# Kernel tuning notes

Measured on AMD Instinct MI355X. Metric: run time of the kernel, lower is better.

The kernel has to match this reference:

```python
import jax, jax.numpy as jnp
import numpy as np

HIDDEN = 1024
HEADS = 16
HEAD_DIM = HIDDEN // HEADS
EPS = 1e-6


def _layernorm(x, gamma, beta):
    mu = jnp.mean(x, axis=-1, keepdims=True)
    var = jnp.mean(jnp.square(x - mu), axis=-1, keepdims=True)
    return (x - mu) * jax.lax.rsqrt(var + EPS) * gamma + beta


def setup_inputs() -> dict:
    key = jax.random.key(0)
    ks = jax.random.split(key, 16)
    B, S, D = 2, 2048, HIDDEN
    s = 1.0 / np.sqrt(D)
    inp = {
        "x": jax.random.normal(ks[0], (B, S, D), dtype=jnp.float32),
        "Wq": jax.random.uniform(ks[1], (D, D), jnp.float32, -s, s),
        "bq": jnp.zeros((D,), jnp.float32),
        "Wk": jax.random.uniform(ks[2], (D, D), jnp.float32, -s, s),
        "bk": jnp.zeros((D,), jnp.float32),
        "Wv": jax.random.uniform(ks[3], (D, D), jnp.float32, -s, s),
        "bv": jnp.zeros((D,), jnp.float32),
        "Wo": jax.random.uniform(ks[4], (D, D), jnp.float32, -s, s),
        "bo": jnp.zeros((D,), jnp.float32),
        "g1": jnp.ones((D,), jnp.float32),
        "b1": jnp.zeros((D,), jnp.float32),
        "Wup": jax.random.uniform(ks[5], (D, 4 * D), jnp.float32, -s, s),
        "bup": jnp.zeros((4 * D,), jnp.float32),
        "Wdn": jax.random.uniform(ks[6], (4 * D, D), jnp.float32, -0.5 * s, 0.5 * s),
        "bdn": jnp.zeros((D,), jnp.float32),
        "g2": jnp.ones((D,), jnp.float32),
        "b2": jnp.zeros((D,), jnp.float32),
    }
    return inp


def _forward(x, Wq, bq, Wk, bk, Wv, bv, Wo, bo, g1, b1, Wup, bup, Wdn, bdn, g2, b2):
    B, S, D = x.shape
    H, Hd = HEADS, HEAD_DIM
    # projections -> (B, H, S, Hd)
    q = (x @ Wq + bq).reshape(B, S, H, Hd).transpose(0, 2, 1, 3)
    k = (x @ Wk + bk).reshape(B, S, H, Hd).transpose(0, 2, 1, 3)
    v = (x @ Wv + bv).reshape(B, S, H, Hd).transpose(0, 2, 1, 3)
    # full NxN scores (faithful to the source: explicit QK^T, mask, softmax, AV)
    scores = jnp.einsum("bhqd,bhkd->bhqk", q, k) / np.sqrt(Hd)
    causal = jnp.tril(jnp.ones((S, S), dtype=bool))  # (S, S)
    scores = jnp.where(causal, scores, jnp.float32(-1e20))
    attn = jax.nn.softmax(scores, axis=-1)
    # dropout is identity in eval mode
    mid = jnp.einsum("bhqk,bhkd->bqhd", attn, v).reshape(B, S, D)
    attn_out = mid @ Wo + bo
    x = _layernorm(x + attn_out, g1, b1)
    # FFN
    up = jax.nn.relu(x @ Wup + bup)
    down = up @ Wdn + bdn
    return _layernorm(x + down, g2, b2)


def reference(x, Wq, bq, Wk, bk, Wv, bv, Wo, bo, g1, b1, Wup, bup, Wdn, bdn, g2, b2):
    return _forward(x, Wq, bq, Wk, bk, Wv, bv, Wo, bo, g1, b1, Wup, bup, Wdn, bdn, g2, b2)
```

## Files before the change

### kernel.cpp

```cpp
#include <hip/hip_runtime.h>

#define D_MODEL 1024
#define D_FFN   4096
#define SEQ     2048
#define NROWS   4096
#define QKV_LD  3072

typedef __bf16 bf16x8 __attribute__((ext_vector_type(8)));
typedef float  floatx4 __attribute__((ext_vector_type(4)));

#define MFMA_BF16 __builtin_amdgcn_mfma_f32_16x16x32_bf16

__device__ __forceinline__ unsigned short f2bf(float f) {
  unsigned int u = __float_as_uint(f);
  u += 0x7FFFu + ((u >> 16) & 1u);
  return (unsigned short)(u >> 16);
}

template <int C>
__device__ __forceinline__ float ror16(float x) {
  return __int_as_float(
      __builtin_amdgcn_mov_dpp(__float_as_int(x), 0x120 | C, 0xf, 0xf, true));
}

__device__ __forceinline__ void async16(const unsigned short* g, unsigned short* l) {
  __builtin_amdgcn_global_load_lds(
      (const __attribute__((address_space(1))) unsigned int*)g,
      (__attribute__((address_space(3))) unsigned int*)l, 16, 0, 0);
}

__global__ __launch_bounds__(256) void k_prep(
    const float* __restrict__ x,
    const float* __restrict__ Wq, const float* __restrict__ Wk,
    const float* __restrict__ Wv, const float* __restrict__ Wo,
    const float* __restrict__ Wup, const float* __restrict__ Wdn,
    const float* __restrict__ bq, const float* __restrict__ bk,
    const float* __restrict__ bv,
    unsigned short* __restrict__ x_bf, unsigned short* __restrict__ WqkvT,
    unsigned short* __restrict__ WoT, unsigned short* __restrict__ WupT,
    unsigned short* __restrict__ WdnT, float* __restrict__ bqkv) {
  __shared__ float tile[32][33];
  int b = blockIdx.x;
  if (b < 4096) {
    long i = ((long)b * 256 + threadIdx.x) * 4;
    float4 v = *(const float4*)(x + i);
    ushort4 o;
    o.x = f2bf(v.x); o.y = f2bf(v.y); o.z = f2bf(v.z); o.w = f2bf(v.w);
    *(ushort4*)(x_bf + i) = o;
    return;
  }
  if (b >= 16384) {
    int i = (b - 16384) * 256 + threadIdx.x;
    if (i < 3072) {
      float v = (i < 1024) ? bq[i] : (i < 2048) ? bk[i - 1024] : bv[i - 2048];
      bqkv[i] = v;
    }
    return;
  }
  const float* W; unsigned short* WT; int R, C, bx, by;
  if (b < 8192) {
    int z = (b - 4096) >> 10, idx = (b - 4096) & 1023;
    W = (z == 0) ? Wq : (z == 1) ? Wk : (z == 2) ? Wv : Wo;
    WT = (z < 3) ? (WqkvT + (size_t)z * D_MODEL * D_MODEL) : WoT;
    R = D_MODEL; C = D_MODEL; bx = idx & 31; by = idx >> 5;
  } else if (b < 12288) {
    int idx = b - 8192;
    W = Wup; WT = WupT; R = D_MODEL; C = D_FFN; bx = idx & 127; by = idx >> 7;
  } else {
    int idx = b - 12288;
    W = Wdn; WT = WdnT; R = D_FFN; C = D_MODEL; bx = idx & 31; by = idx >> 5;
  }
  int tx = threadIdx.x & 31, ty = threadIdx.x >> 5;
  long gx = (long)bx * 32, gy = (long)by * 32;
  #pragma unroll
  for (int j = 0; j < 4; j++)
    tile[ty + j * 8][tx] = W[(gy + ty + j * 8) * C + gx + tx];
  __syncthreads();
  #pragma unroll
  for (int j = 0; j < 4; j++)
    WT[(gx + ty + j * 8) * R + gy + tx] = f2bf(tile[tx][ty + j * 8]);
}

__global__ __launch_bounds__(512, 2) void k_gemm128(
    const unsigned short* __restrict__ A,
    const unsigned short* __restrict__ Bt,
    const float* __restrict__ bias,
    void* __restrict__ Cp, unsigned short* __restrict__ VtOut,
    int M, int N, int K, int flags, int rx, int ry) {
  __shared__ unsigned short lds[2 * 16384];
  int tid = threadIdx.x, lane = tid & 63, wave = tid >> 6;
  int quad = lane >> 4, l16 = lane & 15;
  int wm = wave >> 2, wn = wave & 3;

  int nx = gridDim.x, ny = gridDim.y;
  int orig = blockIdx.y * nx + blockIdx.x;
  int xcd = orig & 7;
  int s = orig >> 3;
  int mr = nx / rx, mc = ny / ry;
  int rr = xcd / ry, rc = xcd % ry;
  int im = s % mr, in_ = s / mr;
  long bm = (long)(rr * mr + im) * 128;
  long bn = (long)(rc * mc + in_) * 128;

  int T = K / 64;

  const floatx4 fz = {0.f, 0.f, 0.f, 0.f};
  floatx4 acc[4][2];
  #pragma unroll
  for (int i = 0; i < 4; i++)
    #pragma unroll
    for (int j = 0; j < 2; j++) acc[i][j] = fz;

  int srow = tid >> 3;
  int sc = (tid & 7) ^ (srow & 7);
  const unsigned short* Ag = A + (bm + srow) * (long)K + sc * 8;
  const unsigned short* Bg = Bt + (bn + srow) * (long)K + sc * 8;

  auto stage = [&](int tt, int c) {
    unsigned short* An = lds + c * 16384;
    unsigned short* Bn = An + 8192;
    long ko = (long)tt * 64;
    async16(Ag + ko, An + wave * 512);
    async16(Ag + 64 * (long)K + ko, An + 4096 + wave * 512);
    async16(Bg + ko, Bn + wave * 512);
    async16(Bg + 64 * (long)K + ko, Bn + 4096 + wave * 512);
  };

  int aoff = (wm * 64 + l16) * 64;
  int boff = (wn * 32 + l16) * 64;
  int sw = l16 & 7;
  int ca0 = (quad ^ sw) * 8;
  int ca1 = ((4 + quad) ^ sw) * 8;

  stage(0, 0);
  for (int t = 0; t < T; t++) {
    int c = t & 1;
    const unsigned short* Ac = lds + c * 16384;
    const unsigned short* Bc = Ac + 8192;
    int tn = (t + 1 < T) ? t + 1 : T - 1;
    stage(tn, c ^ 1);
    __asm__ volatile("s_waitcnt vmcnt(4)" ::: "memory");
    __builtin_amdgcn_s_barrier();

    bf16x8 af0[4], bf0[2], af1[4], bf1[2];
    #pragma unroll
    for (int m = 0; m < 4; m++) af0[m] = *(const bf16x8*)(Ac + aoff + m * 1024 + ca0);
    #pragma unroll
    for (int n = 0; n < 2; n++) bf0[n] = *(const bf16x8*)(Bc + boff + n * 1024 + ca0);
    #pragma unroll
    for (int m = 0; m < 4; m++) af1[m] = *(const bf16x8*)(Ac + aoff + m * 1024 + ca1);
    #pragma unroll
    for (int n = 0; n < 2; n++) bf1[n] = *(const bf16x8*)(Bc + boff + n * 1024 + ca1);
    #pragma unroll
    for (int m = 0; m < 4; m++)
      #pragma unroll
      for (int n = 0; n < 2; n++)
        acc[m][n] = MFMA_BF16(af0[m], bf0[n], acc[m][n], 0, 0, 0);
    #pragma unroll
    for (int m = 0; m < 4; m++)
      #pragma unroll
      for (int n = 0; n < 2; n++)
        acc[m][n] = MFMA_BF16(af1[m], bf1[n], acc[m][n], 0, 0, 0);
    __builtin_amdgcn_s_barrier();
  }

  bool f32out = (flags & 1) != 0;
  bool relu   = (flags & 2) != 0;
  bool vtr    = (flags & 4) != 0 && bn >= 2048;
  if (f32out) {
    float* outf = (float*)Cp;
    #pragma unroll
    for (int n = 0; n < 2; n++) {
      long col = bn + wn * 32 + n * 16 + l16;
      float bvv = bias[col];
      #pragma unroll
      for (int m = 0; m < 4; m++) {
        long row = bm + wm * 64 + m * 16 + quad * 4;
        #pragma unroll
        for (int r = 0; r < 4; r++) {
          float v = acc[m][n][r] + bvv;
          if (relu) v = fmaxf(v, 0.0f);
          outf[(row + r) * (long)N + col] = v;
        }
      }
    }
  } else if (vtr) {
    __asm__ volatile("s_waitcnt vmcnt(0)" ::: "memory");
    __syncthreads();
    unsigned short* lwT = lds + wave * 2304;
    #pragma unroll
    for (int n = 0; n < 2; n++) {
      long col = bn + wn * 32 + n * 16 + l16;
      float bvv = bias[col];
      ushort4 u;
      #pragma unroll
      for (int m = 0; m < 4; m++) {
        u.x = f2bf(acc[m][0 + n][0] + bvv);
        u.y = f2bf(acc[m][n][1] + bvv);
        u.z = f2bf(acc[m][n][2] + bvv);
        u.w = f2bf(acc[m][n][3] + bvv);
        *(ushort4*)(lwT + (n * 16 + l16) * 72 + m * 16 + quad * 4) = u;
      }
    }
    __syncthreads();
    long d0 = bn - 2048 + wn * 32;
    long grow = bm + wm * 64;
    int rseg = (lane & 7) * 8;
    #pragma unroll
    for (int k = 0; k < 4; k++) {
      int cl = k * 8 + (lane >> 3);
      bf16x8 vv = *(const bf16x8*)(lwT + cl * 72 + rseg);
      *(bf16x8*)(VtOut + (d0 + cl) * (long)NROWS + grow + rseg) = vv;
    }
  } else {
    __asm__ volatile("s_waitcnt vmcnt(0)" ::: "memory");
    __syncthreads();
    unsigned short* outh = (unsigned short*)Cp;
    unsigned short* lw = lds + wave * 2560;
    #pragma unroll
    for (int n = 0; n < 2; n++) {
      long col = bn + wn * 32 + n * 16 + l16;
      float bvv = bias[col];
      #pragma unroll
      for (int m = 0; m < 4; m++) {
        #pragma unroll
        for (int r = 0; r < 4; r++) {
          float v = acc[m][n][r] + bvv;
          if (relu) v = fmaxf(v, 0.0f);
          lw[(m * 16 + quad * 4 + r) * 40 + n * 16 + l16] = f2bf(v);
        }
      }
    }
    int rrb = lane >> 2;
    int c8 = (lane & 3) * 8;
    long grow = bm + wm * 64;
    long gcol = bn + wn * 32 + c8;
    #pragma unroll
    for (int k = 0; k < 4; k++) {
      int rw = rrb + k * 16;
      bf16x8 vv = *(const bf16x8*)(lw + rw * 40 + c8);
      *(bf16x8*)(outh + (grow + rw) * (long)N + gcol) = vv;
    }
  }
}

#define PLD 72
__global__ __launch_bounds__(256) void k_attn(
    const unsigned short* __restrict__ QKV,
    const unsigned short* __restrict__ Vt,
    unsigned short* __restrict__ Omat) {
  __shared__ unsigned short Ks[64 * 64];
  __shared__ unsigned short Vs[64 * 64];
  __shared__ unsigned short Ps[4][16 * PLD];
  int tid = threadIdx.x;
  int lane = tid & 63, wave = tid >> 6;
  int quad = lane >> 4, l16 = lane & 15;
  int z = blockIdx.x;
  int bh = z & 31;
  int qt = 31 - (z >> 5);
  int b = bh >> 4, h = bh & 15;
  long rowbase = (long)b * SEQ;
  int hd0 = h * 64;
  unsigned short* pw = &Ps[wave][0];
  const float SCL = 0.18033688f;
  const floatx4 fz = {0.f, 0.f, 0.f, 0.f};

  int r_in = lane >> 3;
  int cpos = lane & 7;

  bf16x8 ones;
  #pragma unroll
  for (int i = 0; i < 8; i++) ones[i] = (__bf16)1.0f;

  int q0w = qt * 64 + wave * 16;
  int qrow = q0w + quad * 4;
  int ntiles = qt + 1;

  bf16x8 qf0, qf1;
  {
    const unsigned short* qp_ =
        QKV + (rowbase + q0w + l16) * (long)QKV_LD + hd0 + quad * 8;
    qf0 = *(const bf16x8*)(qp_);
    qf1 = *(const bf16x8*)(qp_ + 32);
  }

  floatx4 ao[4], aol;
  #pragma unroll
  for (int t = 0; t < 4; t++) ao[t] = fz;
  aol = fz;
  float m_i[4];
  #pragma unroll
  for (int r = 0; r < 4; r++) m_i[r] = -3.0e38f;

  for (int it = 0; it < ntiles; it++) {
    int kv0 = it << 6;
    #pragma unroll
    for (int jj = 0; jj < 2; jj++) {
      int j = wave * 2 + jj;
      int r = j * 8 + r_in;
      int c = cpos ^ (r & 7);
      const unsigned short* gk =
          QKV + (rowbase + kv0 + r) * (long)QKV_LD + 1024 + hd0 + c * 8;
      async16(gk, Ks + j * 512);
      const unsigned short* gv =
          Vt + (long)(hd0 + r) * NROWS + rowbase + kv0 + c * 8;
      async16(gv, Vs + j * 512);
    }
    __syncthreads();

    floatx4 sacc[4];
    #pragma unroll
    for (int t = 0; t < 4; t++) {
      int row = t * 16 + l16;
      int sw = row & 7;
      bf16x8 kf0 = *(const bf16x8*)(Ks + row * 64 + (quad ^ sw) * 8);
      bf16x8 kf1 = *(const bf16x8*)(Ks + row * 64 + ((quad + 4) ^ sw) * 8);
      sacc[t] = __builtin_amdgcn_mfma_f32_16x16x32_bf16(qf0, kf0, fz, 0, 0, 0);
      sacc[t] = __builtin_amdgcn_mfma_f32_16x16x32_bf16(qf1, kf1, sacc[t], 0, 0, 0);
    }

    if (it == ntiles - 1) {
      #pragma unroll
      for (int t = 0; t < 4; t++) {
        int kvc = kv0 + t * 16 + l16;
        #pragma unroll
        for (int r = 0; r < 4; r++)
          sacc[t][r] = (kvc > qrow + r) ? -1.0e30f : sacc[t][r];
      }
    }

    float Mg = sacc[0][0];
    #pragma unroll
    for (int t = 0; t < 4; t++)
      #pragma unroll
      for (int r = 0; r < 4; r++) Mg = fmaxf(Mg, sacc[t][r]);
    Mg = fmaxf(Mg, ror16<1>(Mg));
    Mg = fmaxf(Mg, ror16<2>(Mg));
    Mg = fmaxf(Mg, ror16<4>(Mg));
    Mg = fmaxf(Mg, ror16<8>(Mg));
    float Mg_s = Mg * SCL;

    float m_min = fminf(fminf(m_i[0], m_i[1]), fminf(m_i[2], m_i[3]));
    if (Mg_s > m_min + 8.0f) {
      #pragma unroll
      for (int r = 0; r < 4; r++) {
        float mn = fmaxf(m_i[r], Mg_s);
        float alpha = __builtin_amdgcn_exp2f(m_i[r] - mn);
        m_i[r] = mn;
        #pragma unroll
        for (int t = 0; t < 4; t++) ao[t][r] *= alpha;
        aol[r] *= alpha;
      }
    }

    #pragma unroll
    for (int t = 0; t < 4; t++)
      #pragma unroll
      for (int r = 0; r < 4; r++) {
        float p = __builtin_amdgcn_exp2f(fmaf(sacc[t][r], SCL, -m_i[r]));
        pw[(quad * 4 + r) * PLD + t * 16 + l16] =
            (unsigned short)(__float_as_uint(p) >> 16);
      }

    __asm__ volatile("s_waitcnt lgkmcnt(0)" ::: "memory");
    bf16x8 pf0 = *(const bf16x8*)(pw + l16 * PLD + quad * 8);
    bf16x8 pf1 = *(const bf16x8*)(pw + l16 * PLD + 32 + quad * 8);

    #pragma unroll
    for (int t = 0; t < 4; t++) {
      int row = t * 16 + l16;
      int sw = row & 7;
      bf16x8 vf0 = *(const bf16x8*)(Vs + row * 64 + (quad ^ sw) * 8);
      bf16x8 vf1 = *(const bf16x8*)(Vs + row * 64 + ((quad + 4) ^ sw) * 8);
      ao[t] = __builtin_amdgcn_mfma_f32_16x16x32_bf16(pf0, vf0, ao[t], 0, 0, 0);
      ao[t] = __builtin_amdgcn_mfma_f32_16x16x32_bf16(pf1, vf1, ao[t], 0, 0, 0);
    }
    aol = __builtin_amdgcn_mfma_f32_16x16x32_bf16(pf0, ones, aol, 0, 0, 0);
    aol = __builtin_amdgcn_mfma_f32_16x16x32_bf16(pf1, ones, aol, 0, 0, 0);

    __syncthreads();
  }

  float inv[4];
  #pragma unroll
  for (int r = 0; r < 4; r++) inv[r] = 1.0f / aol[r];
  #pragma unroll
  for (int t = 0; t < 4; t++)
    #pragma unroll
    for (int r = 0; r < 4; r++)
      Omat[(rowbase + qrow + r) * (long)D_MODEL + hd0 + t * 16 + l16] =
          f2bf(ao[t][r] * inv[r]);
}

__global__ __launch_bounds__(256) void k_add_ln(
    const float* __restrict__ A, const float* __restrict__ P,
    const float* __restrict__ g, const float* __restrict__ be,
    float* __restrict__ Y, unsigned short* __restrict__ Ybf) {
  __shared__ float sb[4], ssb[4];
  int tid = threadIdx.x;
  long base = (long)blockIdx.x * D_MODEL + tid * 4;
  float4 a  = *(const float4*)(A + base);
  float4 p0 = *(const float4*)(P + base);
  float v0 = a.x + p0.x;
  float v1 = a.y + p0.y;
  float v2 = a.z + p0.z;
  float v3 = a.w + p0.w;
  float s  = v0 + v1 + v2 + v3;
  float ss = v0 * v0 + v1 * v1 + v2 * v2 + v3 * v3;
  #pragma unroll
  for (int o = 32; o >= 1; o >>= 1) {
    s  += __shfl_xor(s, o, 64);
    ss += __shfl_xor(ss, o, 64);
  }
  int wave = tid >> 6;
  if ((tid & 63) == 0) { sb[wave] = s; ssb[wave] = ss; }
  __syncthreads();
  s  = sb[0] + sb[1] + sb[2] + sb[3];
  ss = ssb[0] + ssb[1] + ssb[2] + ssb[3];
  float mu  = s * (1.0f / 1024.0f);
  float var = ss * (1.0f / 1024.0f) - mu * mu;
  float rstd = rsqrtf(var + 1e-6f);
  float4 gv  = *(const float4*)(g + tid * 4);
  float4 bev = *(const float4*)(be + tid * 4);
  float o0 = (v0 - mu) * rstd * gv.x + bev.x;
  float o1 = (v1 - mu) * rstd * gv.y + bev.y;
  float o2 = (v2 - mu) * rstd * gv.z + bev.z;
  float o3 = (v3 - mu) * rstd * gv.w + bev.w;
  if (Y) *(float4*)(Y + base) = make_float4(o0, o1, o2, o3);
  if (Ybf) {
    ushort4 u;
    u.x = f2bf(o0); u.y = f2bf(o1); u.z = f2bf(o2); u.w = f2bf(o3);
    *(ushort4*)(Ybf + base) = u;
  }
}

extern "C" void kernel_launch(void* const* d_in, const int* in_sizes, int n_in,
                              void* d_out, int out_size, void* d_ws, size_t ws_size,
                              hipStream_t stream) {
  (void)in_sizes; (void)n_in; (void)out_size; (void)ws_size;
  const float* x   = (const float*)d_in[0];
  const float* Wq  = (const float*)d_in[1];
  const float* bq  = (const float*)d_in[2];
  const float* Wk  = (const float*)d_in[3];
  const float* bk  = (const float*)d_in[4];
  const float* Wv  = (const float*)d_in[5];
  const float* bv  = (const float*)d_in[6];
  const float* Wo  = (const float*)d_in[7];
  const float* bo  = (const float*)d_in[8];
  const float* g1  = (const float*)d_in[9];
  const float* b1  = (const float*)d_in[10];
  const float* Wup = (const float*)d_in[11];
  const float* bup = (const float*)d_in[12];
  const float* Wdn = (const float*)d_in[13];
  const float* bdn = (const float*)d_in[14];
  const float* g2  = (const float*)d_in[15];
  const float* b2  = (const float*)d_in[16];
  float* out = (float*)d_out;

  char* ws = (char*)d_ws;
  size_t off = 0;
  auto alloc = [&](size_t bytes) {
    char* p = ws + off;
    off = (off + bytes + 255) & ~(size_t)255;
    return p;
  };
  unsigned short* x_bf   = (unsigned short*)alloc((size_t)NROWS * D_MODEL * 2);
  unsigned short* WqkvT  = (unsigned short*)alloc((size_t)QKV_LD * D_MODEL * 2);
  unsigned short* WoT    = (unsigned short*)alloc((size_t)D_MODEL * D_MODEL * 2);
  unsigned short* WupT   = (unsigned short*)alloc((size_t)D_FFN * D_MODEL * 2);
  unsigned short* WdnT   = (unsigned short*)alloc((size_t)D_MODEL * D_FFN * 2);
  float*          bqkv   = (float*)alloc((size_t)QKV_LD * 4);
  unsigned short* qkv_bf = (unsigned short*)alloc((size_t)NROWS * QKV_LD * 2);
  unsigned short* Vt     = (unsigned short*)alloc((size_t)D_MODEL * NROWS * 2);
  unsigned short* mid_bf = (unsigned short*)alloc((size_t)NROWS * D_MODEL * 2);
  float*          x1f    = (float*)alloc((size_t)NROWS * D_MODEL * 4);
  unsigned short* x1bf   = (unsigned short*)alloc((size_t)NROWS * D_MODEL * 2);
  float*          part   = (float*)alloc((size_t)NROWS * D_MODEL * 4);
  unsigned short* h_bf   = (unsigned short*)alloc((size_t)NROWS * D_FFN * 2);

  k_prep<<<16396, 256, 0, stream>>>(x, Wq, Wk, Wv, Wo, Wup, Wdn, bq, bk, bv,
                                    x_bf, WqkvT, WoT, WupT, WdnT, bqkv);

  k_gemm128<<<dim3(32, 24), 512, 0, stream>>>(x_bf, WqkvT, bqkv, qkv_bf, Vt,
                                              NROWS, QKV_LD, D_MODEL, 4, 4, 2);

  k_attn<<<1024, 256, 0, stream>>>(qkv_bf, Vt, mid_bf);

  k_gemm128<<<dim3(32, 8), 512, 0, stream>>>(mid_bf, WoT, bo, part, nullptr,
                                             NROWS, D_MODEL, D_MODEL, 1, 4, 2);
  k_add_ln<<<4096, 256, 0, stream>>>(x, part, g1, b1, x1f, x1bf);

  k_gemm128<<<dim3(32, 32), 512, 0, stream>>>(x1bf, WupT, bup, h_bf, nullptr,
                                              NROWS, D_FFN, D_MODEL, 2, 4, 2);
  k_gemm128<<<dim3(32, 8), 512, 0, stream>>>(h_bf, WdnT, bdn, part, nullptr,
                                             NROWS, D_MODEL, D_FFN, 1, 4, 2);
  k_add_ln<<<4096, 256, 0, stream>>>(x1f, part, g2, b2, out, nullptr);
}
```

Before: 318.7 us.

## Pair causal query tiles per block and double-buffer K/V loads in attention

```diff
diff --git a/kernel.cpp b/kernel.cpp
--- a/kernel.cpp
+++ b/kernel.cpp
@@ -249,15 +249,15 @@
     const unsigned short* __restrict__ QKV,
     const unsigned short* __restrict__ Vt,
     unsigned short* __restrict__ Omat) {
-  __shared__ unsigned short Ks[64 * 64];
-  __shared__ unsigned short Vs[64 * 64];
+  __shared__ unsigned short Ks[2][64 * 64];
+  __shared__ unsigned short Vs[2][64 * 64];
   __shared__ unsigned short Ps[4][16 * PLD];
   int tid = threadIdx.x;
   int lane = tid & 63, wave = tid >> 6;
   int quad = lane >> 4, l16 = lane & 15;
   int z = blockIdx.x;
   int bh = z & 31;
-  int qt = 31 - (z >> 5);
+  int qp = z >> 5;
   int b = bh >> 4, h = bh & 15;
   long rowbase = (long)b * SEQ;
   int hd0 = h * 64;
@@ -272,124 +272,143 @@
   #pragma unroll
   for (int i = 0; i < 8; i++) ones[i] = (__bf16)1.0f;
 
-  int q0w = qt * 64 + wave * 16;
-  int qrow = q0w + quad * 4;
-  int ntiles = qt + 1;
-
-  bf16x8 qf0, qf1;
-  {
-    const unsigned short* qp_ =
-        QKV + (rowbase + q0w + l16) * (long)QKV_LD + hd0 + quad * 8;
-    qf0 = *(const bf16x8*)(qp_);
-    qf1 = *(const bf16x8*)(qp_ + 32);
-  }
-
-  floatx4 ao[4], aol;
   #pragma unroll
-  for (int t = 0; t < 4; t++) ao[t] = fz;
-  aol = fz;
-  float m_i[4];
-  #pragma unroll
-  for (int r = 0; r < 4; r++) m_i[r] = -3.0e38f;
-
-  for (int it = 0; it < ntiles; it++) {
-    int kv0 = it << 6;
-    #pragma unroll
-    for (int jj = 0; jj < 2; jj++) {
-      int j = wave * 2 + jj;
-      int r = j * 8 + r_in;
-      int c = cpos ^ (r & 7);
-      const unsigned short* gk =
-          QKV + (rowbase + kv0 + r) * (long)QKV_LD + 1024 + hd0 + c * 8;
-      async16(gk, Ks + j * 512);
-      const unsigned short* gv =
-          Vt + (long)(hd0 + r) * NROWS + rowbase + kv0 + c * 8;
-      async16(gv, Vs + j * 512);
-    }
+  for (int phase = 0; phase < 2; phase++) {
+    int qt = phase ? qp : (31 - qp);
+    int q0w = qt * 64 + wave * 16;
+    int qrow = q0w + quad * 4;
+    int ntiles = qt + 1;
+
+    __asm__ volatile("s_waitcnt vmcnt(0)" ::: "memory");
     __syncthreads();
 
-    floatx4 sacc[4];
-    #pragma unroll
-    for (int t = 0; t < 4; t++) {
-      int row = t * 16 + l16;
-      int sw = row & 7;
-      bf16x8 kf0 = *(const bf16x8*)(Ks + row * 64 + (quad ^ sw) * 8);
-      bf16x8 kf1 = *(const bf16x8*)(Ks + row * 64 + ((quad + 4) ^ sw) * 8);
-      sacc[t] = __builtin_amdgcn_mfma_f32_16x16x32_bf16(qf0, kf0, fz, 0, 0, 0);
-      sacc[t] = __builtin_amdgcn_mfma_f32_16x16x32_bf16(qf1, kf1, sacc[t], 0, 0, 0);
-    }
-
-    if (it == ntiles - 1) {
+    bf16x8 qf0, qf1;
+    {
+      const unsigned short* qp_ =
+          QKV + (rowbase + q0w + l16) * (long)QKV_LD + hd0 + quad * 8;
+      qf0 = *(const bf16x8*)(qp_);
+      qf1 = *(const bf16x8*)(qp_ + 32);
+    }
+    __asm__ volatile("s_waitcnt vmcnt(0)" ::: "memory");
+
+    auto stage = [&](int it, int c) {
+      int kv0 = it << 6;
+      #pragma unroll
+      for (int jj = 0; jj < 2; jj++) {
+        int j = wave * 2 + jj;
+        int r = j * 8 + r_in;
+        int cc = cpos ^ (r & 7);
+        const unsigned short* gk =
+            QKV + (rowbase + kv0 + r) * (long)QKV_LD + 1024 + hd0 + cc * 8;
+        async16(gk, &Ks[c][0] + j * 512);
+        const unsigned short* gv =
+            Vt + (long)(hd0 + r) * NROWS + rowbase + kv0 + cc * 8;
+        async16(gv, &Vs[c][0] + j * 512);
+      }
+    };
+
+    floatx4 ao[4], aol;
+    #pragma unroll
+    for (int t = 0; t < 4; t++) ao[t] = fz;
+    aol = fz;
+    float m_i[4];
+    #pragma unroll
+    for (int r = 0; r < 4; r++) m_i[r] = -3.0e38f;
+
+    stage(0, 0);
+    for (int it = 0; it < ntiles; it++) {
+      int cb = it & 1;
+      int tn = (it + 1 < ntiles) ? it + 1 : ntiles - 1;
+      stage(tn, cb ^ 1);
+      __asm__ volatile("s_waitcnt vmcnt(4)" ::: "memory");
+      __syncthreads();
+      const unsigned short* Kc = &Ks[cb][0];
+      const unsigned short* Vc = &Vs[cb][0];
+      int kv0 = it << 6;
+
+      floatx4 sacc[4];
       #pragma unroll
       for (int t = 0; t < 4; t++) {
-        int kvc = kv0 + t * 16 + l16;
+        int row = t * 16 + l16;
+        int sw = row & 7;
+        bf16x8 kf0 = *(const bf16x8*)(Kc + row * 64 + (quad ^ sw) * 8);
+        bf16x8 kf1 = *(const bf16x8*)(Kc + row * 64 + ((quad + 4) ^ sw) * 8);
+        sacc[t] = __builtin_amdgcn_mfma_f32_16x16x32_bf16(qf0, kf0, fz, 0, 0, 0);
+        sacc[t] = __builtin_amdgcn_mfma_f32_16x16x32_bf16(qf1, kf1, sacc[t], 0, 0, 0);
+      }
+
+      if (it == ntiles - 1) {
         #pragma unroll
-        for (int r = 0; r < 4; r++)
-          sacc[t][r] = (kvc > qrow + r) ? -1.0e30f : sacc[t][r];
-      }
-    }
-
-    float Mg = sacc[0][0];
+        for (int t = 0; t < 4; t++) {
+          int kvc = kv0 + t * 16 + l16;
+          #pragma unroll
+          for (int r = 0; r < 4; r++)
+            sacc[t][r] = (kvc > qrow + r) ? -1.0e30f : sacc[t][r];
+        }
+      }
+
+      float Mg = sacc[0][0];
+      #pragma unroll
+      for (int t = 0; t < 4; t++)
+        #pragma unroll
+        for (int r = 0; r < 4; r++) Mg = fmaxf(Mg, sacc[t][r]);
+      Mg = fmaxf(Mg, ror16<1>(Mg));
+      Mg = fmaxf(Mg, ror16<2>(Mg));
+      Mg = fmaxf(Mg, ror16<4>(Mg));
+      Mg = fmaxf(Mg, ror16<8>(Mg));
+      float Mg_s = Mg * SCL;
+
+      float m_min = fminf(fminf(m_i[0], m_i[1]), fminf(m_i[2], m_i[3]));
+      if (Mg_s > m_min + 8.0f) {
+        #pragma unroll
+        for (int r = 0; r < 4; r++) {
+          float mn = fmaxf(m_i[r], Mg_s);
+          float alpha = __builtin_amdgcn_exp2f(m_i[r] - mn);
+          m_i[r] = mn;
+          #pragma unroll
+          for (int t = 0; t < 4; t++) ao[t][r] *= alpha;
+          aol[r] *= alpha;
+        }
+      }
+
+      #pragma unroll
+      for (int t = 0; t < 4; t++)
+        #pragma unroll
+        for (int r = 0; r < 4; r++) {
+          float p = __builtin_amdgcn_exp2f(fmaf(sacc[t][r], SCL, -m_i[r]));
+          pw[(quad * 4 + r) * PLD + t * 16 + l16] =
+              (unsigned short)(__float_as_uint(p) >> 16);
+        }
+
+      __asm__ volatile("s_waitcnt lgkmcnt(0)" ::: "memory");
+      bf16x8 pf0 = *(const bf16x8*)(pw + l16 * PLD + quad * 8);
+      bf16x8 pf1 = *(const bf16x8*)(pw + l16 * PLD + 32 + quad * 8);
+
+      #pragma unroll
+      for (int t = 0; t < 4; t++) {
+        int row = t * 16 + l16;
+        int sw = row & 7;
+        bf16x8 vf0 = *(const bf16x8*)(Vc + row * 64 + (quad ^ sw) * 8);
+        bf16x8 vf1 = *(const bf16x8*)(Vc + row * 64 + ((quad + 4) ^ sw) * 8);
+        ao[t] = __builtin_amdgcn_mfma_f32_16x16x32_bf16(pf0, vf0, ao[t], 0, 0, 0);
+        ao[t] = __builtin_amdgcn_mfma_f32_16x16x32_bf16(pf1, vf1, ao[t], 0, 0, 0);
+      }
+      aol = __builtin_amdgcn_mfma_f32_16x16x32_bf16(pf0, ones, aol, 0, 0, 0);
+      aol = __builtin_amdgcn_mfma_f32_16x16x32_bf16(pf1, ones, aol, 0, 0, 0);
+
+      __syncthreads();
+    }
+
+    float inv[4];
+    #pragma unroll
+    for (int r = 0; r < 4; r++) inv[r] = 1.0f / aol[r];
     #pragma unroll
     for (int t = 0; t < 4; t++)
       #pragma unroll
-      for (int r = 0; r < 4; r++) Mg = fmaxf(Mg, sacc[t][r]);
-    Mg = fmaxf(Mg, ror16<1>(Mg));
-    Mg = fmaxf(Mg, ror16<2>(Mg));
-    Mg = fmaxf(Mg, ror16<4>(Mg));
-    Mg = fmaxf(Mg, ror16<8>(Mg));
-    float Mg_s = Mg * SCL;
-
-    float m_min = fminf(fminf(m_i[0], m_i[1]), fminf(m_i[2], m_i[3]));
-    if (Mg_s > m_min + 8.0f) {
-      #pragma unroll
-      for (int r = 0; r < 4; r++) {
-        float mn = fmaxf(m_i[r], Mg_s);
-        float alpha = __builtin_amdgcn_exp2f(m_i[r] - mn);
-        m_i[r] = mn;
-        #pragma unroll
-        for (int t = 0; t < 4; t++) ao[t][r] *= alpha;
-        aol[r] *= alpha;
-      }
-    }
-
-    #pragma unroll
-    for (int t = 0; t < 4; t++)
-      #pragma unroll
-      for (int r = 0; r < 4; r++) {
-        float p = __builtin_amdgcn_exp2f(fmaf(sacc[t][r], SCL, -m_i[r]));
-        pw[(quad * 4 + r) * PLD + t * 16 + l16] =
-            (unsigned short)(__float_as_uint(p) >> 16);
-      }
-
-    __asm__ volatile("s_waitcnt lgkmcnt(0)" ::: "memory");
-    bf16x8 pf0 = *(const bf16x8*)(pw + l16 * PLD + quad * 8);
-    bf16x8 pf1 = *(const bf16x8*)(pw + l16 * PLD + 32 + quad * 8);
-
-    #pragma unroll
-    for (int t = 0; t < 4; t++) {
-      int row = t * 16 + l16;
-      int sw = row & 7;
-      bf16x8 vf0 = *(const bf16x8*)(Vs + row * 64 + (quad ^ sw) * 8);
-      bf16x8 vf1 = *(const bf16x8*)(Vs + row * 64 + ((quad + 4) ^ sw) * 8);
-      ao[t] = __builtin_amdgcn_mfma_f32_16x16x32_bf16(pf0, vf0, ao[t], 0, 0, 0);
-      ao[t] = __builtin_amdgcn_mfma_f32_16x16x32_bf16(pf1, vf1, ao[t], 0, 0, 0);
-    }
-    aol = __builtin_amdgcn_mfma_f32_16x16x32_bf16(pf0, ones, aol, 0, 0, 0);
-    aol = __builtin_amdgcn_mfma_f32_16x16x32_bf16(pf1, ones, aol, 0, 0, 0);
-
-    __syncthreads();
-  }
-
-  float inv[4];
-  #pragma unroll
-  for (int r = 0; r < 4; r++) inv[r] = 1.0f / aol[r];
-  #pragma unroll
-  for (int t = 0; t < 4; t++)
-    #pragma unroll
-    for (int r = 0; r < 4; r++)
-      Omat[(rowbase + qrow + r) * (long)D_MODEL + hd0 + t * 16 + l16] =
-          f2bf(ao[t][r] * inv[r]);
+      for (int r = 0; r < 4; r++)
+        Omat[(rowbase + qrow + r) * (long)D_MODEL + hd0 + t * 16 + l16] =
+            f2bf(ao[t][r] * inv[r]);
+  }
 }
 
 __global__ __launch_bounds__(256) void k_add_ln(
@@ -484,7 +503,7 @@
   k_gemm128<<<dim3(32, 24), 512, 0, stream>>>(x_bf, WqkvT, bqkv, qkv_bf, Vt,
                                               NROWS, QKV_LD, D_MODEL, 4, 4, 2);
 
-  k_attn<<<1024, 256, 0, stream>>>(qkv_bf, Vt, mid_bf);
+  k_attn<<<512, 256, 0, stream>>>(qkv_bf, Vt, mid_bf);
 
   k_gemm128<<<dim3(32, 8), 512, 0, stream>>>(mid_bf, WoT, bo, part, nullptr,
                                              NROWS, D_MODEL, D_MODEL, 1, 4, 2);
```

Measured after the change: 333.3 us. 4.6% more time.
